# Performance work log

Measured on AMD Instinct MI355X. Metric: run time of the kernel, lower is better.

The kernel has to match this reference:

```python
import jax, jax.numpy as jnp
import numpy as np

EPS_S = 1e-06
EPS_R = 1e-06

def _gaussian_masks(mu, logsx, logsy, rho, H, W, dtype):
    # coordinate grid in [-1,1], grid[h,w] = (x, y)
    ys = jnp.linspace(-1.0, 1.0, H, dtype=dtype)
    xs = jnp.linspace(-1.0, 1.0, W, dtype=dtype)
    Y, X = jnp.meshgrid(ys, xs, indexing='ij')  # [H,W]
    sx = jnp.exp(logsx)[:, None, None] + EPS_S   # [n,1,1]
    sy = jnp.exp(logsy)[:, None, None] + EPS_S
    r = jnp.tanh(rho)[:, None, None]
    xc = (X[None] - mu[:, 0, None, None]) / sx   # [n,H,W]
    yc = (Y[None] - mu[:, 1, None, None]) / sy
    A = xc ** 2 + yc ** 2 - 2.0 * r * xc * yc
    denom = 2.0 * (1.0 - r ** 2 + EPS_R)
    return jnp.exp(-A / denom)                   # [n,H,W]

def setup_inputs() -> dict:
    key = jax.random.key(0)
    ks = jax.random.split(key, 6)
    B, C, H, W, n = 32, 256, 36, 64, 4096
    feat = jax.random.normal(ks[0], (B, C, H, W), dtype=jnp.float32)
    mu = jax.random.uniform(ks[1], (n, 2), dtype=jnp.float32) * 2.0 - 1.0
    logsx = jnp.zeros((n,), dtype=jnp.float32)
    logsy = jnp.zeros((n,), dtype=jnp.float32)
    rho = jnp.zeros((n,), dtype=jnp.float32)
    weight = jax.random.normal(ks[5], (n, C), dtype=jnp.float32) * 0.01
    return {"feat": feat, "mu": mu, "logsx": logsx, "logsy": logsy, "rho": rho, "weight": weight}

def reference(feat, mu, logsx, logsy, rho, weight):
    B, C, H, W = feat.shape
    G = _gaussian_masks(mu, logsx, logsy, rho, H, W, feat.dtype)  # [n,H,W]
    # pooled[b,n,c] = sum_{h,w} feat[b,c,h,w] * G[n,h,w]  (batched GEMM)
    pooled = jnp.einsum('bchw,nhw->bnc', feat, G)
    out = jnp.einsum('bnc,nc->bn', pooled, weight.astype(feat.dtype))
    return out
```

## Files before the change

### kernel.cpp

```cpp
#include <hip/hip_runtime.h>
#include <hip/hip_bf16.h>

#define P_HW   2304
#define NG     4096
#define NCOL   8192
#define KDIM   P_HW

typedef __bf16 bf16x8 __attribute__((ext_vector_type(8)));
typedef float  f32x4  __attribute__((ext_vector_type(4)));

__device__ __forceinline__ unsigned short f2bf(float f) {
    union { float f; unsigned int u; } x; x.f = f;
    unsigned int r = x.u + 0x7FFFu + ((x.u >> 16) & 1u);
    return (unsigned short)(r >> 16);
}

__global__ __launch_bounds__(256) void prep_kernel(
    const float* __restrict__ feat,
    const float* __restrict__ mu,
    const float* __restrict__ logsx,
    const float* __restrict__ logsy,
    const float* __restrict__ rho,
    unsigned short* __restrict__ F,
    unsigned short* __restrict__ G,
    float* __restrict__ out) {
    const int bid = blockIdx.x;
    const int tid = threadIdx.x;
    if (bid < 9216) {
        const size_t i = ((size_t)bid * 256 + tid) * 8;
        const float4 v0 = *(const float4*)(feat + i);
        const float4 v1 = *(const float4*)(feat + i + 4);
        union { unsigned short s[8]; uint4 q; } o;
        o.s[0] = f2bf(v0.x); o.s[1] = f2bf(v0.y); o.s[2] = f2bf(v0.z); o.s[3] = f2bf(v0.w);
        o.s[4] = f2bf(v1.x); o.s[5] = f2bf(v1.y); o.s[6] = f2bf(v1.z); o.s[7] = f2bf(v1.w);
        *(uint4*)(F + i) = o.q;
    } else if (bid < 13312) {
        const int n = bid - 9216;
        const float mux = mu[2 * n], muy = mu[2 * n + 1];
        const float sx = __expf(logsx[n]) + 1e-6f;
        const float sy = __expf(logsy[n]) + 1e-6f;
        const float r  = tanhf(rho[n]);
        const float inv_den = 1.0f / (2.0f * (1.0f - r * r + 1e-6f));
        const float isx = 1.0f / sx, isy = 1.0f / sy;
        for (int base = tid * 8; base < P_HW; base += 2048) {
            const int h = base >> 6, w0 = base & 63;
            const float Y  = -1.0f + (float)h * (2.0f / 35.0f);
            const float yc = (Y - muy) * isy;
            union { unsigned short s[8]; uint4 q; } o;
#pragma unroll
            for (int j = 0; j < 8; ++j) {
                const float X  = -1.0f + (float)(w0 + j) * (2.0f / 63.0f);
                const float xc = (X - mux) * isx;
                const float A  = xc * xc + yc * yc - 2.0f * r * xc * yc;
                o.s[j] = f2bf(__expf(-A * inv_den));
            }
            *(uint4*)&G[(size_t)n * P_HW + base] = o.q;
        }
    } else {
        const size_t i = ((size_t)(bid - 13312) * 256 + tid) * 8;
        const float4 z = {0.f, 0.f, 0.f, 0.f};
        *(float4*)(out + i)     = z;
        *(float4*)(out + i + 4) = z;
    }
}

__device__ __forceinline__ void async16(const void* g, void* l) {
    __builtin_amdgcn_global_load_lds(
        (__attribute__((address_space(1))) void*)(unsigned long long)g,
        (__attribute__((address_space(3))) void*)(unsigned int)(unsigned long long)l,
        16, 0, 0);
}

__global__ __launch_bounds__(128, 2) void gemm_fused(
    const unsigned short* __restrict__ G,
    const unsigned short* __restrict__ F,
    const float* __restrict__ weight,
    float* __restrict__ out)
{
    __shared__ __align__(16) unsigned short ldsA[128 * 64];
    __shared__ __align__(16) unsigned short ldsB[128 * 64];

    const int tid  = threadIdx.x;
    const int lane = tid & 63;
    const int wave = tid >> 6;
    const int quad = lane >> 4, m = lane & 15;

    const int rowBase = blockIdx.y * 128;
    const int colBase = blockIdx.x * 128;

    const int r0 = tid >> 3;
    const int c0 = (tid & 7) ^ (r0 & 7);
    const unsigned short* Aptr0 = G + (size_t)(rowBase + r0) * KDIM + c0 * 8;
    const unsigned short* Bptr0 = F + (size_t)(colBase + r0) * KDIM + c0 * 8;
    const int lds0 = tid * 8;

    f32x4 acc[4][8];
#pragma unroll
    for (int i = 0; i < 4; ++i)
#pragma unroll
        for (int j = 0; j < 8; ++j)
            acc[i][j] = (f32x4){0.f, 0.f, 0.f, 0.f};

    for (int k0 = 0; k0 < KDIM; k0 += 64) {
#pragma unroll
        for (int i = 0; i < 8; ++i)
            async16(Aptr0 + k0 + i * 16 * KDIM, &ldsA[lds0 + i * 1024]);
#pragma unroll
        for (int i = 0; i < 8; ++i)
            async16(Bptr0 + k0 + i * 16 * KDIM, &ldsB[lds0 + i * 1024]);
        __syncthreads();

#pragma unroll
        for (int h = 0; h < 2; ++h) {
            bf16x8 a[4], b[8];
#pragma unroll
            for (int i = 0; i < 4; ++i) {
                const int r  = wave * 64 + i * 16 + m;
                const int cp = (h * 4 + quad) ^ (r & 7);
                a[i] = *(const bf16x8*)&ldsA[r * 64 + cp * 8];
            }
#pragma unroll
            for (int j = 0; j < 8; ++j) {
                const int r  = j * 16 + m;
                const int cp = (h * 4 + quad) ^ (r & 7);
                b[j] = *(const bf16x8*)&ldsB[r * 64 + cp * 8];
            }
#pragma unroll
            for (int i = 0; i < 4; ++i)
#pragma unroll
                for (int j = 0; j < 8; ++j)
                    acc[i][j] = __builtin_amdgcn_mfma_f32_16x16x32_bf16(a[i], b[j], acc[i][j], 0, 0, 0);
        }
        __syncthreads();
    }

    const int bidx   = colBase >> 8;
    const int cwbase = (colBase & 255) + m;
#pragma unroll
    for (int i = 0; i < 4; ++i) {
#pragma unroll
        for (int reg = 0; reg < 4; ++reg) {
            const int n = rowBase + wave * 64 + i * 16 + quad * 4 + reg;
            const float* wrow = weight + (size_t)n * 256 + cwbase;
            float s = 0.f;
#pragma unroll
            for (int j = 0; j < 8; ++j)
                s += acc[i][j][reg] * wrow[j * 16];
            s += __shfl_xor(s, 1);
            s += __shfl_xor(s, 2);
            s += __shfl_xor(s, 4);
            s += __shfl_xor(s, 8);
            if (m == 0)
                atomicAdd(out + (size_t)bidx * NG + n, s);
        }
    }
}

extern "C" void kernel_launch(void* const* d_in, const int* in_sizes, int n_in,
                              void* d_out, int out_size, void* d_ws, size_t ws_size,
                              hipStream_t stream) {
    const float* feat   = (const float*)d_in[0];
    const float* mu     = (const float*)d_in[1];
    const float* logsx  = (const float*)d_in[2];
    const float* logsy  = (const float*)d_in[3];
    const float* rho    = (const float*)d_in[4];
    const float* weight = (const float*)d_in[5];
    float* out = (float*)d_out;

    unsigned short* Gbuf = (unsigned short*)d_ws;
    unsigned short* Fbuf = Gbuf + (size_t)NG * P_HW;

    hipLaunchKernelGGL(prep_kernel, dim3(13376), dim3(256), 0, stream,
                       feat, mu, logsx, logsy, rho, Fbuf, Gbuf, out);

    hipLaunchKernelGGL(gemm_fused, dim3(NCOL / 128, NG / 128), dim3(128), 0, stream,
                       Gbuf, Fbuf, weight, out);
}
```

Before: 276.8 us.

## Rewrite GEMM as 256x256 tile, 8-wave kernel with 4-stage async LDS pipeline

The fused GEMM moves from 128x128 tiles with 2 waves and a single-buffered 64-wide K loop to 256x256 tiles with 8 waves (2x4 wave grid). It runs a 4-slot circular LDS buffer with 32-wide K steps, issuing global-to-LDS loads three steps ahead, and interleaves LDS reads, async loads and MFMA bursts using explicit barriers, waitcnts and setprio. The epilogue reduces the four column-waves' partial sums through LDS and writes each output once, since each block now covers one full batch's 256 channels, so the atomics go away. This is meant to raise data reuse and hide load latency, at the cost of 128KB of LDS and heavy register use. That may limit occupancy, and the hand-written waitcnt scheduling is fragile.

```diff
diff --git a/kernel.cpp b/kernel.cpp
--- a/kernel.cpp
+++ b/kernel.cpp
@@ -5,6 +5,7 @@
 #define NG     4096
 #define NCOL   8192
 #define KDIM   P_HW
+#define NT     72
 
 typedef __bf16 bf16x8 __attribute__((ext_vector_type(8)));
 typedef float  f32x4  __attribute__((ext_vector_type(4)));
@@ -71,88 +72,134 @@
         16, 0, 0);
 }
 
-__global__ __launch_bounds__(128, 2) void gemm_fused(
+__global__ __launch_bounds__(512, 2) void gemm_fused(
     const unsigned short* __restrict__ G,
     const unsigned short* __restrict__ F,
     const float* __restrict__ weight,
     float* __restrict__ out)
 {
-    __shared__ __align__(16) unsigned short ldsA[128 * 64];
-    __shared__ __align__(16) unsigned short ldsB[128 * 64];
+    __shared__ __align__(16) unsigned short lds[4 * 16384];
 
     const int tid  = threadIdx.x;
     const int lane = tid & 63;
-    const int wave = tid >> 6;
+    const int wid  = tid >> 6;
+    const int wr   = wid >> 2;
+    const int wc   = wid & 3;
     const int quad = lane >> 4, m = lane & 15;
 
-    const int rowBase = blockIdx.y * 128;
-    const int colBase = blockIdx.x * 128;
-
-    const int r0 = tid >> 3;
-    const int c0 = (tid & 7) ^ (r0 & 7);
-    const unsigned short* Aptr0 = G + (size_t)(rowBase + r0) * KDIM + c0 * 8;
-    const unsigned short* Bptr0 = F + (size_t)(colBase + r0) * KDIM + c0 * 8;
-    const int lds0 = tid * 8;
-
-    f32x4 acc[4][8];
-#pragma unroll
-    for (int i = 0; i < 4; ++i)
-#pragma unroll
-        for (int j = 0; j < 8; ++j)
+    const int rowBase = blockIdx.y * 256;
+    const int colBase = blockIdx.x * 256;
+
+    const int rA = tid >> 2;
+    const int cA = (tid & 3) ^ (rA & 3);
+    const unsigned short* pA = G + (size_t)(rowBase + rA) * KDIM + cA * 8;
+    const unsigned short* pB = F + (size_t)(colBase + rA) * KDIM + cA * 8;
+
+    const int sw   = (quad ^ (m & 3)) * 8;
+    const int aoff = (wr * 128 + m) * 32 + sw;
+    const int boff = (wc * 64  + m) * 32 + sw;
+
+    f32x4 acc[8][4];
+#pragma unroll
+    for (int i = 0; i < 8; ++i)
+#pragma unroll
+        for (int j = 0; j < 4; ++j)
             acc[i][j] = (f32x4){0.f, 0.f, 0.f, 0.f};
 
-    for (int k0 = 0; k0 < KDIM; k0 += 64) {
-#pragma unroll
-        for (int i = 0; i < 8; ++i)
-            async16(Aptr0 + k0 + i * 16 * KDIM, &ldsA[lds0 + i * 1024]);
-#pragma unroll
-        for (int i = 0; i < 8; ++i)
-            async16(Bptr0 + k0 + i * 16 * KDIM, &ldsB[lds0 + i * 1024]);
-        __syncthreads();
-
-#pragma unroll
-        for (int h = 0; h < 2; ++h) {
-            bf16x8 a[4], b[8];
-#pragma unroll
-            for (int i = 0; i < 4; ++i) {
-                const int r  = wave * 64 + i * 16 + m;
-                const int cp = (h * 4 + quad) ^ (r & 7);
-                a[i] = *(const bf16x8*)&ldsA[r * 64 + cp * 8];
-            }
-#pragma unroll
-            for (int j = 0; j < 8; ++j) {
-                const int r  = j * 16 + m;
-                const int cp = (h * 4 + quad) ^ (r & 7);
-                b[j] = *(const bf16x8*)&ldsB[r * 64 + cp * 8];
-            }
-#pragma unroll
-            for (int i = 0; i < 4; ++i)
-#pragma unroll
-                for (int j = 0; j < 8; ++j)
-                    acc[i][j] = __builtin_amdgcn_mfma_f32_16x16x32_bf16(a[i], b[j], acc[i][j], 0, 0, 0);
-        }
-        __syncthreads();
-    }
-
-    const int bidx   = colBase >> 8;
-    const int cwbase = (colBase & 255) + m;
-#pragma unroll
-    for (int i = 0; i < 4; ++i) {
+#pragma unroll
+    for (int t = 0; t < 3; ++t) {
+        const int bo = t * 16384;
+#pragma unroll
+        for (int i = 0; i < 2; ++i)
+            async16(pA + t * 32 + i * (128 * KDIM), &lds[bo + i * 4096 + tid * 8]);
+#pragma unroll
+        for (int i = 0; i < 2; ++i)
+            async16(pB + t * 32 + i * (128 * KDIM), &lds[bo + 8192 + i * 4096 + tid * 8]);
+    }
+    asm volatile("s_waitcnt vmcnt(8)" ::: "memory");
+    __builtin_amdgcn_s_barrier();
+
+    for (int t = 0; t < NT; ++t) {
+        const int bo  = (t & 3) * 16384;
+        const int w   = (t + 3 >= NT) ? (t + 3 - NT) : (t + 3);
+        const int wbo = (w & 3) * 16384;
+        const unsigned short* pAw = pA + w * 32;
+        const unsigned short* pBw = pB + w * 32;
+
+        bf16x8 a[4], b[4];
+#pragma unroll
+        for (int i = 0; i < 4; ++i)
+            a[i] = *(const bf16x8*)&lds[bo + aoff + i * 512];
+#pragma unroll
+        for (int j = 0; j < 4; ++j)
+            b[j] = *(const bf16x8*)&lds[bo + 8192 + boff + j * 512];
+#pragma unroll
+        for (int i = 0; i < 2; ++i)
+            async16(pAw + i * (128 * KDIM), &lds[wbo + i * 4096 + tid * 8]);
+        __builtin_amdgcn_sched_barrier(0);
+        __builtin_amdgcn_s_barrier();
+        asm volatile("s_waitcnt lgkmcnt(0)" ::: "memory");
+        __builtin_amdgcn_sched_barrier(0);
+        __builtin_amdgcn_s_setprio(1);
+#pragma unroll
+        for (int i = 0; i < 4; ++i)
+#pragma unroll
+            for (int j = 0; j < 4; ++j)
+                acc[i][j] = __builtin_amdgcn_mfma_f32_16x16x32_bf16(a[i], b[j], acc[i][j], 0, 0, 0);
+        __builtin_amdgcn_s_setprio(0);
+        __builtin_amdgcn_sched_barrier(0);
+        __builtin_amdgcn_s_barrier();
+        __builtin_amdgcn_sched_barrier(0);
+#pragma unroll
+        for (int i = 0; i < 4; ++i)
+            a[i] = *(const bf16x8*)&lds[bo + aoff + (i + 4) * 512];
+#pragma unroll
+        for (int i = 0; i < 2; ++i)
+            async16(pBw + i * (128 * KDIM), &lds[wbo + 8192 + i * 4096 + tid * 8]);
+        __builtin_amdgcn_sched_barrier(0);
+        __builtin_amdgcn_s_barrier();
+        asm volatile("s_waitcnt lgkmcnt(0)" ::: "memory");
+        __builtin_amdgcn_sched_barrier(0);
+        __builtin_amdgcn_s_setprio(1);
+#pragma unroll
+        for (int i = 0; i < 4; ++i)
+#pragma unroll
+            for (int j = 0; j < 4; ++j)
+                acc[i + 4][j] = __builtin_amdgcn_mfma_f32_16x16x32_bf16(a[i], b[j], acc[i + 4][j], 0, 0, 0);
+        __builtin_amdgcn_s_setprio(0);
+        asm volatile("s_waitcnt vmcnt(8)" ::: "memory");
+        __builtin_amdgcn_sched_barrier(0);
+        __builtin_amdgcn_s_barrier();
+        __builtin_amdgcn_sched_barrier(0);
+    }
+
+    asm volatile("s_waitcnt vmcnt(0)" ::: "memory");
+    __syncthreads();
+
+    float* red = (float*)lds;
+    const int cwbase = wc * 64 + m;
+#pragma unroll
+    for (int i = 0; i < 8; ++i) {
 #pragma unroll
         for (int reg = 0; reg < 4; ++reg) {
-            const int n = rowBase + wave * 64 + i * 16 + quad * 4 + reg;
-            const float* wrow = weight + (size_t)n * 256 + cwbase;
+            const int nloc = wr * 128 + i * 16 + quad * 4 + reg;
+            const float* wrow = weight + (size_t)(rowBase + nloc) * 256 + cwbase;
             float s = 0.f;
 #pragma unroll
-            for (int j = 0; j < 8; ++j)
+            for (int j = 0; j < 4; ++j)
                 s += acc[i][j][reg] * wrow[j * 16];
             s += __shfl_xor(s, 1);
             s += __shfl_xor(s, 2);
             s += __shfl_xor(s, 4);
             s += __shfl_xor(s, 8);
             if (m == 0)
-                atomicAdd(out + (size_t)bidx * NG + n, s);
+                red[wc * 256 + nloc] = s;
         }
+    }
+    __syncthreads();
+    if (tid < 256) {
+        const float s = red[tid] + red[256 + tid] + red[512 + tid] + red[768 + tid];
+        out[(size_t)blockIdx.x * NG + rowBase + tid] = s;
     }
 }
 
@@ -173,6 +220,6 @@
     hipLaunchKernelGGL(prep_kernel, dim3(13376), dim3(256), 0, stream,
                        feat, mu, logsx, logsy, rho, Fbuf, Gbuf, out);
 
-    hipLaunchKernelGGL(gemm_fused, dim3(NCOL / 128, NG / 128), dim3(128), 0, stream,
+    hipLaunchKernelGGL(gemm_fused, dim3(NCOL / 256, NG / 256), dim3(512), 0, stream,
                        Gbuf, Fbuf, weight, out);
 }
```

After: 286.6 us. 3.5% more time.
